# Kernel optimization log

Measured on AMD Instinct MI355X. Metric: run time of the kernel, lower is better.

The kernel has to match this reference:

```python
import jax, jax.numpy as jnp
import numpy as np

N, IN_DIM = 50000, 1024
E = 100000
NUM_REL = 40
HEADS, OUT_DIM = 4, 200
HID = HEADS * OUT_DIM  # 800
B = 8192
NEG_SLOPE = 0.2


def setup_inputs() -> dict:
    key = jax.random.key(0)
    ks = jax.random.split(key, 12)
    node_emb = jax.random.normal(ks[0], (N, IN_DIM), dtype=jnp.float32)
    # RelGAT learnable params
    W = jax.random.normal(ks[1], (IN_DIM, HID), dtype=jnp.float32) * (1.0 / np.sqrt(IN_DIM))
    bias = jnp.zeros((HID,), dtype=jnp.float32)
    a_src = jax.random.normal(ks[2], (HEADS, OUT_DIM), dtype=jnp.float32) * 0.1
    a_dst = jax.random.normal(ks[3], (HEADS, OUT_DIM), dtype=jnp.float32) * 0.1
    a_rel = jax.random.normal(ks[4], (HEADS, OUT_DIM), dtype=jnp.float32) * 0.1
    rel_feat = jax.random.normal(ks[5], (NUM_REL, HID), dtype=jnp.float32) * 0.1
    # DistMult scorer relation embeddings
    rel_emb = jax.random.normal(ks[6], (NUM_REL, HID), dtype=jnp.float32) * 0.1
    # Graph structure (constants)
    edge_index = jax.random.randint(ks[7], (2, E), 0, N, dtype=jnp.int64)
    edge_type = jax.random.randint(ks[8], (E,), 0, NUM_REL, dtype=jnp.int64)
    # Triple batch
    src_ids = jax.random.randint(ks[9], (B,), 0, N, dtype=jnp.int64)
    rel_ids = jax.random.randint(ks[10], (B,), 0, NUM_REL, dtype=jnp.int64)
    dst_ids = jax.random.randint(ks[11], (B,), 0, N, dtype=jnp.int64)
    return dict(node_emb=node_emb, W=W, bias=bias, a_src=a_src, a_dst=a_dst,
                a_rel=a_rel, rel_feat=rel_feat, rel_emb=rel_emb,
                edge_index=edge_index, edge_type=edge_type,
                src_ids=src_ids, rel_ids=rel_ids, dst_ids=dst_ids)


def _rel_gat(node_emb, W, bias, a_src, a_dst, a_rel, rel_feat, edge_index, edge_type):
    src, dst = edge_index[0], edge_index[1]
    h = (node_emb @ W).reshape(N, HEADS, OUT_DIM)          # [N,H,D]
    hs = h[src]                                            # [E,H,D] gather
    hd = h[dst]                                            # [E,H,D] gather
    r = rel_feat[edge_type].reshape(E, HEADS, OUT_DIM)     # [E,H,D]
    # relation-conditioned attention logits per head
    logits = (jnp.einsum('ehd,hd->eh', hs, a_src)
              + jnp.einsum('ehd,hd->eh', hd, a_dst)
              + jnp.einsum('ehd,hd->eh', r, a_rel))        # [E,H]
    logits = jax.nn.leaky_relu(logits, NEG_SLOPE)
    # segment softmax over incoming edges of each destination node
    seg_max = jax.ops.segment_max(logits, dst, num_segments=N)   # [N,H]
    e = jnp.exp(logits - seg_max[dst])                           # [E,H]
    denom = jax.ops.segment_sum(e, dst, num_segments=N)          # [N,H]
    alpha = e / denom[dst]                                       # [E,H]
    # weighted scatter-aggregate of source messages
    out = jax.ops.segment_sum(alpha[:, :, None] * hs, dst, num_segments=N)  # [N,H,D]
    return out.reshape(N, HID) + bias                            # dropout: eval mode (identity)


def reference(node_emb, W, bias, a_src, a_dst, a_rel, rel_feat, rel_emb,
              edge_index, edge_type, src_ids, rel_ids, dst_ids):
    refined = _rel_gat(node_emb, W, bias, a_src, a_dst, a_rel, rel_feat,
                       edge_index, edge_type)                # [N, HID]
    src_vec = refined[src_ids]                               # [B, HID]
    dst_vec = refined[dst_ids]                               # [B, HID]
    # DistMult: sum(s * r * d)
    scores = jnp.sum(src_vec * rel_emb[rel_ids] * dst_vec, axis=-1)  # [B]
    return scores
```

## Files before the change

kernel.cpp:

```cpp
#include <hip/hip_runtime.h>
#include <hip/hip_bf16.h>
#include <math.h>

#define NN 50000
#define IN_DIM 1024
#define EE 100000
#define NUM_REL 40
#define HEADS 4
#define OUT_D 200
#define HID 800
#define BB 8192
#define SLOT_CAP 16384
#define SRC_CAP 50176
#define WT_COLS 896

typedef __attribute__((ext_vector_type(8))) short short8;
typedef __attribute__((ext_vector_type(4))) float f32x4;

__device__ inline unsigned short f2bf(float f) {
    unsigned int u = __float_as_uint(f);
    u += 0x7FFF + ((u >> 16) & 1);
    return (unsigned short)(u >> 16);
}
__device__ inline float bf2f(unsigned short s) {
    return __uint_as_float(((unsigned int)s) << 16);
}
__device__ inline void gl2lds16(const unsigned short* g, unsigned short* l) {
    __builtin_amdgcn_global_load_lds(
        (const __attribute__((address_space(1))) void*)g,
        (__attribute__((address_space(3))) void*)l, 16, 0, 0);
}

#define INIT_BLOCKS 196
__global__ __launch_bounds__(256) void k_init_wa(int* slot_of_node, int* xrow_of_node,
                                                 int* deg, int* counters,
                                                 const float* W, const float* a_src,
                                                 const float* a_dst, const float* a_rel,
                                                 const float* rel_feat, float* Wa, float* prel) {
    int b = blockIdx.x;
    if (b < INIT_BLOCKS) {
        int i = b * 256 + threadIdx.x;
        if (i < NN) { slot_of_node[i] = -1; xrow_of_node[i] = -1; }
        if (i < SLOT_CAP) deg[i] = 0;
        if (i < 8) counters[i] = 0;
        return;
    }
    int wid = (b - INIT_BLOCKS) * 4 + (threadIdx.x >> 6);
    int lane = threadIdx.x & 63;
    if (wid >= IN_DIM * 8 + NUM_REL * HEADS) return;
    float acc = 0.f;
    int d = lane * 4;
    if (d < OUT_D) {
        const float* row;
        const float* a;
        if (wid < IN_DIM * 8) {
            int k = wid >> 3, c = wid & 7;
            int h = c & 3;
            row = W + (size_t)k * HID + h * OUT_D;
            a = ((c < 4) ? a_src : a_dst) + h * OUT_D;
        } else {
            int j = wid - IN_DIM * 8;
            int r = j >> 2, h = j & 3;
            row = rel_feat + (size_t)r * HID + h * OUT_D;
            a = a_rel + h * OUT_D;
        }
        float4 wv = *(const float4*)(row + d);
        float4 av = *(const float4*)(a + d);
        acc = wv.x * av.x + wv.y * av.y + wv.z * av.z + wv.w * av.w;
    }
    for (int off = 32; off; off >>= 1) acc += __shfl_down(acc, off, 64);
    if (lane == 0) {
        if (wid < IN_DIM * 8) Wa[wid] = acc;
        else prel[wid - IN_DIM * 8] = acc;
    }
}

__global__ void k_build_slots(const int* src_ids, const int* dst_ids,
                              int* slot_of_node, int* counters, int* scorelist) {
    int i = blockIdx.x * 256 + threadIdx.x;
    if (i >= 2 * BB) return;
    int n = (i < BB) ? src_ids[i] : dst_ids[i - BB];
    if (slot_of_node[n] == -1) {
        if (atomicCAS(&slot_of_node[n], -1, -2) == -1) {
            int s = atomicAdd(&counters[0], 1);
            slot_of_node[n] = s;
            scorelist[s] = n;
        }
    }
}

__global__ void k_edge0(const int* ei, const int* slot_of_node,
                        int* xrow_of_node, int* counters, int* rows, int* deg) {
    int e = blockIdx.x * 256 + threadIdx.x;
    if (e >= EE) return;
    int dn = ei[EE + e];
    int slot = slot_of_node[dn];
    if (slot < 0) return;
    int sn = ei[e];
    if (xrow_of_node[sn] == -1) {
        if (atomicCAS(&xrow_of_node[sn], -1, -2) == -1) {
            int t = atomicAdd(&counters[1], 1);
            rows[t] = sn;
            xrow_of_node[sn] = t;
        }
    }
    atomicAdd(&deg[slot], 1);
}

__global__ __launch_bounds__(256) void k_tail_scan(const int* scorelist, int* xrow_of_node,
                                                   int* counters, int* rows,
                                                   const int* deg, int* base, int* cursor) {
    int t = threadIdx.x;
    if (blockIdx.x == 0) {
        __shared__ int pref[257];
        int s = 0;
        const int4* dv = (const int4*)(deg + t * (SLOT_CAP / 256));
        for (int i = 0; i < SLOT_CAP / 256 / 4; ++i) {
            int4 v = dv[i];
            s += v.x + v.y + v.z + v.w;
        }
        pref[t + 1] = s;
        if (t == 0) pref[0] = 0;
        __syncthreads();
        if (t == 0)
            for (int i = 1; i <= 256; ++i) pref[i] += pref[i - 1];
        __syncthreads();
        int r = pref[t];
        for (int i = 0; i < SLOT_CAP / 256; ++i) {
            int idx = t * (SLOT_CAP / 256) + i;
            base[idx] = r;
            cursor[idx] = r;
            r += deg[idx];
        }
        return;
    }
    int i = (blockIdx.x - 1) * 256 + t;
    if (i >= counters[0]) return;
    int n = scorelist[i];
    if (xrow_of_node[n] < 0) {
        int tt = atomicAdd(&counters[3], 1);
        int xr = counters[1] + tt;
        xrow_of_node[n] = xr;
        rows[xr] = n;
    }
}

#define WT_BLOCKS 224
__global__ __launch_bounds__(256) void k_gather_wt(const float* x, const int* rows,
                                                   const int* counters, unsigned short* xg,
                                                   const float* W, const float* Wa,
                                                   unsigned short* Wt) {
    int t = threadIdx.x;
    if (blockIdx.x < WT_BLOCKS) {
        __shared__ float tile[64][65];
        int b = blockIdx.x;
        int k0 = (b & 15) * 64, c0 = (b >> 4) * 64;
        {
            int kk = t >> 2, cc = (t & 3) * 16;
            for (int i = 0; i < 16; ++i) {
                int c = c0 + cc + i;
                float v = 0.f;
                if (c < HID) v = W[(size_t)(k0 + kk) * HID + c];
                else if (c < HID + 8) v = Wa[(size_t)(k0 + kk) * 8 + (c - HID)];
                tile[cc + i][kk] = v;
            }
        }
        __syncthreads();
        {
            int cc = t >> 2, kk = (t & 3) * 16;
            unsigned short o[16];
            for (int i = 0; i < 16; ++i) o[i] = f2bf(tile[cc][kk + i]);
            *(short8*)(Wt + (size_t)(c0 + cc) * IN_DIM + k0 + kk) = *(short8*)o;
            *(short8*)(Wt + (size_t)(c0 + cc) * IN_DIM + k0 + kk + 8) = *(short8*)(o + 8);
        }
        return;
    }
    int nneed = counters[1] + counters[3];
    int gid = (blockIdx.x - WT_BLOCKS) * 256 + t;
    int row = gid >> 7;
    if (row >= nneed) return;
    int j = (gid & 127) * 8;
    int node = rows[row];
    const float* src = x + (size_t)node * IN_DIM + j;
    float4 a = *(const float4*)(src);
    float4 b = *(const float4*)(src + 4);
    unsigned short o[8] = {f2bf(a.x), f2bf(a.y), f2bf(a.z), f2bf(a.w),
                           f2bf(b.x), f2bf(b.y), f2bf(b.z), f2bf(b.w)};
    *(short8*)(xg + (size_t)row * IN_DIM + j) = *(short8*)o;
}

#define GBM 128
#define GBN 128
#define GBK 64
__global__ __launch_bounds__(256) void k_hgemm(const unsigned short* xg, const unsigned short* Wt,
                                               const int* counters, unsigned short* h_src,
                                               float* sS, float* sD) {
    int nsrc = counters[1];
    int nneed = nsrc + counters[3];
    int col0 = blockIdx.x * GBN;
    int row0 = blockIdx.y * GBM;
    int rowlim = (col0 == 768) ? nneed : nsrc;
    if (row0 >= rowlim) return;
    __shared__ unsigned short As[GBM * GBK];
    __shared__ unsigned short Bs[GBN * GBK];
    int t = threadIdx.x;
    int crow = ((t >> 6) << 4) + (t & 15), coff = ((t >> 4) & 3) << 3;
    const unsigned short* a0 = xg + (size_t)(row0 + crow) * IN_DIM + coff;
    const unsigned short* a1 = a0 + (size_t)64 * IN_DIM;
    const unsigned short* b0 = Wt + (size_t)(col0 + crow) * IN_DIM + coff;
    const unsigned short* b1 = b0 + (size_t)64 * IN_DIM;
    unsigned short* la0 = As + t * 8;
    unsigned short* la1 = As + (256 + t) * 8;
    unsigned short* la2 = As + (512 + t) * 8;
    unsigned short* la3 = As + (768 + t) * 8;
    unsigned short* lb0 = Bs + t * 8;
    unsigned short* lb1 = Bs + (256 + t) * 8;
    unsigned short* lb2 = Bs + (512 + t) * 8;
    unsigned short* lb3 = Bs + (768 + t) * 8;
    int w = t >> 6, lane = t & 63;
    int ga = (w >> 1) * 4, gb = (w & 1) * 4;
    int wr = (w >> 1) * 64, wc = (w & 1) * 64;
    int fm = lane & 15, fq = lane >> 4;
    f32x4 acc[4][4] = {};
    for (int k0 = 0; k0 < IN_DIM; k0 += GBK) {
        __syncthreads();
        gl2lds16(a0 + k0, la0);
        gl2lds16(a1 + k0, la1);
        gl2lds16(a0 + k0 + 32, la2);
        gl2lds16(a1 + k0 + 32, la3);
        gl2lds16(b0 + k0, lb0);
        gl2lds16(b1 + k0, lb1);
        gl2lds16(b0 + k0 + 32, lb2);
        gl2lds16(b1 + k0 + 32, lb3);
        __syncthreads();
#pragma unroll
        for (int s = 0; s < 2; ++s) {
            short8 af[4], bf[4];
#pragma unroll
            for (int i = 0; i < 4; ++i)
                af[i] = *(const short8*)&As[(s * 512 + (ga + i) * 64 + lane) * 8];
#pragma unroll
            for (int j = 0; j < 4; ++j)
                bf[j] = *(const short8*)&Bs[(s * 512 + (gb + j) * 64 + lane) * 8];
#pragma unroll
            for (int i = 0; i < 4; ++i)
#pragma unroll
                for (int j = 0; j < 4; ++j)
                    acc[i][j] = __builtin_amdgcn_mfma_f32_16x16x32_bf16(af[i], bf[j], acc[i][j], 0, 0, 0);
        }
    }
#pragma unroll
    for (int i = 0; i < 4; ++i) {
#pragma unroll
        for (int j = 0; j < 4; ++j) {
            int gcol = col0 + wc + j * 16 + fm;
            if (gcol >= HID + 8) continue;
#pragma unroll
            for (int r = 0; r < 4; ++r) {
                int grow = row0 + wr + i * 16 + fq * 4 + r;
                float v = acc[i][j][r];
                if (gcol < HID) {
                    if (grow < nsrc) h_src[(size_t)grow * HID + gcol] = f2bf(v);
                } else if (grow < nneed) {
                    int c = gcol - HID;
                    if (c < 4) sS[grow * 4 + c] = v;
                    else sD[grow * 4 + (c - 4)] = v;
                }
            }
        }
    }
}

__global__ void k_place(const int* ei, const int* etype, const int* slot_of_node,
                        const int* xrow_of_node, int* cursor,
                        const float* sS, const float* sD, const float* prel,
                        float* clogit, int* tlist) {
    int e = blockIdx.x * 256 + threadIdx.x;
    if (e >= EE) return;
    int dn = ei[EE + e];
    int slot = slot_of_node[dn];
    if (slot < 0) return;
    int sn = ei[e];
    int r = etype[e];
    int xs = xrow_of_node[sn];
    int xd = xrow_of_node[dn];
    int pos = atomicAdd(&cursor[slot], 1);
    tlist[pos] = xs;
    float4 lg;
    float* lp = (float*)&lg;
#pragma unroll
    for (int h = 0; h < 4; ++h) {
        float v = sS[xs * 4 + h] + sD[xd * 4 + h] + prel[r * 4 + h];
        lp[h] = v > 0.f ? v : 0.2f * v;
    }
    *(float4*)&clogit[(size_t)pos * 4] = lg;
}

__global__ __launch_bounds__(256) void k_aggregate(const int* counters, const int* base,
                                                   const int* deg, const int* tlist,
                                                   const float* clogit,
                                                   const unsigned short* h_src, const float* bias,
                                                   float* refined) {
    int b = blockIdx.x;
    if (b >= counters[0]) return;
    int beg = base[b], d = deg[b];
    __shared__ float m4[4], den4[4];
    __shared__ float alpha[64][4];
    __shared__ int tsl[64];
    int t = threadIdx.x;
    if (t < 4) {
        float m = -3e38f;
        for (int j = 0; j < d; ++j)
            m = fmaxf(m, clogit[(size_t)(beg + j) * 4 + t]);
        float s = 0.f;
        for (int j = 0; j < d; ++j)
            s += expf(clogit[(size_t)(beg + j) * 4 + t] - m);
        m4[t] = m;
        den4[t] = s;
    }
    __syncthreads();
    int h0 = t / 200, h1 = (t + 256) / 200, h2 = (t + 512) / 200;
    float acc0 = 0.f, acc1 = 0.f, acc2 = 0.f, acc3 = 0.f;
    for (int j0 = 0; j0 < d; j0 += 64) {
        int nc = min(64, d - j0);
        if (t < nc * 4) {
            int j = t >> 2, h = t & 3;
            alpha[j][h] = expf(clogit[(size_t)(beg + j0 + j) * 4 + h] - m4[h]) / den4[h];
            if (h == 0) tsl[j] = tlist[beg + j0 + j];
        }
        __syncthreads();
        for (int j = 0; j < nc; ++j) {
            const unsigned short* hr = h_src + (size_t)tsl[j] * HID;
            acc0 += alpha[j][h0] * bf2f(hr[t]);
            acc1 += alpha[j][h1] * bf2f(hr[t + 256]);
            acc2 += alpha[j][h2] * bf2f(hr[t + 512]);
            if (t < 32) acc3 += alpha[j][3] * bf2f(hr[768 + t]);
        }
        __syncthreads();
    }
    float* rr = refined + (size_t)b * HID;
    rr[t] = acc0 + bias[t];
    rr[t + 256] = acc1 + bias[t + 256];
    rr[t + 512] = acc2 + bias[t + 512];
    if (t < 32) rr[768 + t] = acc3 + bias[768 + t];
}

__global__ __launch_bounds__(256) void k_score(const int* src_ids, const int* rel_ids,
                                               const int* dst_ids, const int* slot_of_node,
                                               const float* rel_emb, const float* refined,
                                               float* out) {
    int gid = blockIdx.x * 256 + threadIdx.x;
    int b = gid >> 6;
    int lane = threadIdx.x & 63;
    if (b >= BB) return;
    int ss = slot_of_node[src_ids[b]];
    int ds = slot_of_node[dst_ids[b]];
    int r = rel_ids[b];
    const float* sv = refined + (size_t)ss * HID;
    const float* dv = refined + (size_t)ds * HID;
    const float* rv = rel_emb + (size_t)r * HID;
    float acc = 0.f;
    for (int c4 = lane; c4 < 200; c4 += 64) {
        float4 s = *(const float4*)(sv + c4 * 4);
        float4 dq = *(const float4*)(dv + c4 * 4);
        float4 rr = *(const float4*)(rv + c4 * 4);
        acc += s.x * rr.x * dq.x + s.y * rr.y * dq.y + s.z * rr.z * dq.z + s.w * rr.w * dq.w;
    }
    for (int off = 32; off; off >>= 1) acc += __shfl_down(acc, off, 64);
    if (lane == 0) out[b] = acc;
}

extern "C" void kernel_launch(void* const* d_in, const int* in_sizes, int n_in,
                              void* d_out, int out_size, void* d_ws, size_t ws_size,
                              hipStream_t stream) {
    const float* node_emb = (const float*)d_in[0];
    const float* W        = (const float*)d_in[1];
    const float* bias     = (const float*)d_in[2];
    const float* a_src    = (const float*)d_in[3];
    const float* a_dst    = (const float*)d_in[4];
    const float* a_rel    = (const float*)d_in[5];
    const float* rel_feat = (const float*)d_in[6];
    const float* rel_emb  = (const float*)d_in[7];
    const int* edge_index = (const int*)d_in[8];
    const int* edge_type  = (const int*)d_in[9];
    const int* src_ids    = (const int*)d_in[10];
    const int* rel_ids    = (const int*)d_in[11];
    const int* dst_ids    = (const int*)d_in[12];
    float* out = (float*)d_out;

    char* w = (char*)d_ws;
    auto alloc = [&](size_t bytes) -> void* {
        void* p = (void*)w;
        w += (bytes + 255) & ~(size_t)255;
        return p;
    };
    int* slot_of_node = (int*)alloc((size_t)NN * 4);
    int* xrow_of_node = (int*)alloc((size_t)NN * 4);
    int* scorelist    = (int*)alloc((size_t)SLOT_CAP * 4);
    int* rows         = (int*)alloc((size_t)NN * 4);
    int* counters     = (int*)alloc(256);
    int* deg          = (int*)alloc((size_t)SLOT_CAP * 4);
    int* base         = (int*)alloc((size_t)SLOT_CAP * 4);
    int* cursor       = (int*)alloc((size_t)SLOT_CAP * 4);
    int* tlist        = (int*)alloc((size_t)EE * 4);
    float* clogit = (float*)alloc((size_t)EE * 4 * 4);
    float* sS     = (float*)alloc((size_t)SRC_CAP * 4 * 4);
    float* sD     = (float*)alloc((size_t)SRC_CAP * 4 * 4);
    float* Wa     = (float*)alloc((size_t)IN_DIM * 8 * 4);
    float* prel   = (float*)alloc((size_t)NUM_REL * 4 * 4);
    unsigned short* xg    = (unsigned short*)alloc((size_t)SRC_CAP * IN_DIM * 2);
    unsigned short* Wt    = (unsigned short*)alloc((size_t)WT_COLS * IN_DIM * 2);
    unsigned short* h_src = (unsigned short*)alloc((size_t)SRC_CAP * HID * 2);
    float* refined = (float*)alloc((size_t)SLOT_CAP * HID * 4);

    int wa_blocks = (IN_DIM * 8 + NUM_REL * HEADS + 3) / 4;
    k_init_wa<<<INIT_BLOCKS + wa_blocks, 256, 0, stream>>>(
        slot_of_node, xrow_of_node, deg, counters,
        W, a_src, a_dst, a_rel, rel_feat, Wa, prel);
    k_build_slots<<<(2 * BB + 255) / 256, 256, 0, stream>>>(src_ids, dst_ids, slot_of_node,
                                                            counters, scorelist);
    k_edge0<<<(EE + 255) / 256, 256, 0, stream>>>(edge_index, slot_of_node,
                                                  xrow_of_node, counters, rows, deg);
    k_tail_scan<<<1 + SLOT_CAP / 256, 256, 0, stream>>>(scorelist, xrow_of_node, counters,
                                                        rows, deg, base, cursor);
    k_gather_wt<<<WT_BLOCKS + (NN * 128) / 256, 256, 0, stream>>>(
        node_emb, rows, counters, xg, W, Wa, Wt);
    dim3 ggrid(WT_COLS / GBN, (SRC_CAP + GBM - 1) / GBM);
    k_hgemm<<<ggrid, 256, 0, stream>>>(xg, Wt, counters, h_src, sS, sD);
    k_place<<<(EE + 255) / 256, 256, 0, stream>>>(edge_index, edge_type, slot_of_node,
                                                  xrow_of_node, cursor, sS, sD, prel,
                                                  clogit, tlist);
    k_aggregate<<<SLOT_CAP, 256, 0, stream>>>(counters, base, deg, tlist,
                                              clogit, h_src, bias, refined);
    k_score<<<(BB * 64 + 255) / 256, 256, 0, stream>>>(src_ids, rel_ids, dst_ids,
                                                       slot_of_node, rel_emb, refined, out);
}
```

Baseline: 519.0 us.

## Aggregate atomics per wave, grid-stride gather, and swizzle GEMM tile order

Replaces the per-thread atomicAdd on the global counters with a wave-level ballot and prefix scheme, so one lane reserves indices for the whole wave. This cuts contention on the counters in the slot-building, edge and tail kernels. The row gather now uses a fixed grid of 3584 blocks with a grid-stride loop instead of launching blocks for all 50000 possible rows. The GEMM block index is remapped into groups of 8 row tiles across all column tiles to improve L2 reuse of A tiles. Index assignment order becomes wave-ordered, which changes row numbering but not the final values.

```diff
diff --git a/kernel.cpp b/kernel.cpp
--- a/kernel.cpp
+++ b/kernel.cpp
@@ -29,6 +29,17 @@
     __builtin_amdgcn_global_load_lds(
         (const __attribute__((address_space(1))) void*)g,
         (__attribute__((address_space(3))) void*)l, 16, 0, 0);
+}
+
+__device__ inline int wave_compact(bool won, int* ctr) {
+    unsigned long long m = __ballot(won);
+    if (!m) return -1;
+    int lane = threadIdx.x & 63;
+    int leader = __ffsll((long long)m) - 1;
+    int base = 0;
+    if (lane == leader) base = atomicAdd(ctr, __popcll(m));
+    base = __shfl(base, leader, 64);
+    return won ? base + __popcll(m & ((1ull << lane) - 1)) : -1;
 }
 
 #define INIT_BLOCKS 196
@@ -78,33 +89,43 @@
 __global__ void k_build_slots(const int* src_ids, const int* dst_ids,
                               int* slot_of_node, int* counters, int* scorelist) {
     int i = blockIdx.x * 256 + threadIdx.x;
-    if (i >= 2 * BB) return;
-    int n = (i < BB) ? src_ids[i] : dst_ids[i - BB];
-    if (slot_of_node[n] == -1) {
-        if (atomicCAS(&slot_of_node[n], -1, -2) == -1) {
-            int s = atomicAdd(&counters[0], 1);
-            slot_of_node[n] = s;
-            scorelist[s] = n;
-        }
+    bool valid = i < 2 * BB;
+    int n = 0;
+    bool won = false;
+    if (valid) {
+        n = (i < BB) ? src_ids[i] : dst_ids[i - BB];
+        if (slot_of_node[n] == -1)
+            won = (atomicCAS(&slot_of_node[n], -1, -2) == -1);
+    }
+    int s = wave_compact(won, &counters[0]);
+    if (won) {
+        slot_of_node[n] = s;
+        scorelist[s] = n;
     }
 }
 
 __global__ void k_edge0(const int* ei, const int* slot_of_node,
                         int* xrow_of_node, int* counters, int* rows, int* deg) {
     int e = blockIdx.x * 256 + threadIdx.x;
-    if (e >= EE) return;
-    int dn = ei[EE + e];
-    int slot = slot_of_node[dn];
-    if (slot < 0) return;
-    int sn = ei[e];
-    if (xrow_of_node[sn] == -1) {
-        if (atomicCAS(&xrow_of_node[sn], -1, -2) == -1) {
-            int t = atomicAdd(&counters[1], 1);
-            rows[t] = sn;
-            xrow_of_node[sn] = t;
-        }
-    }
-    atomicAdd(&deg[slot], 1);
+    bool valid = e < EE;
+    int slot = -1, sn = 0;
+    if (valid) {
+        int dn = ei[EE + e];
+        slot = slot_of_node[dn];
+    }
+    bool surv = valid && slot >= 0;
+    bool won = false;
+    if (surv) {
+        sn = ei[e];
+        if (xrow_of_node[sn] == -1)
+            won = (atomicCAS(&xrow_of_node[sn], -1, -2) == -1);
+    }
+    int t = wave_compact(won, &counters[1]);
+    if (won) {
+        rows[t] = sn;
+        xrow_of_node[sn] = t;
+    }
+    if (surv) atomicAdd(&deg[slot], 1);
 }
 
 __global__ __launch_bounds__(256) void k_tail_scan(const int* scorelist, int* xrow_of_node,
@@ -135,10 +156,15 @@
         return;
     }
     int i = (blockIdx.x - 1) * 256 + t;
-    if (i >= counters[0]) return;
-    int n = scorelist[i];
-    if (xrow_of_node[n] < 0) {
-        int tt = atomicAdd(&counters[3], 1);
+    bool valid = i < counters[0];
+    int n = 0;
+    bool won = false;
+    if (valid) {
+        n = scorelist[i];
+        won = (xrow_of_node[n] < 0);
+    }
+    int tt = wave_compact(won, &counters[3]);
+    if (won) {
         int xr = counters[1] + tt;
         xrow_of_node[n] = xr;
         rows[xr] = n;
@@ -146,6 +172,7 @@
 }
 
 #define WT_BLOCKS 224
+#define GATHER_BLOCKS 3584
 __global__ __launch_bounds__(256) void k_gather_wt(const float* x, const int* rows,
                                                    const int* counters, unsigned short* xg,
                                                    const float* W, const float* Wa,
@@ -176,17 +203,19 @@
         return;
     }
     int nneed = counters[1] + counters[3];
-    int gid = (blockIdx.x - WT_BLOCKS) * 256 + t;
-    int row = gid >> 7;
-    if (row >= nneed) return;
-    int j = (gid & 127) * 8;
-    int node = rows[row];
-    const float* src = x + (size_t)node * IN_DIM + j;
-    float4 a = *(const float4*)(src);
-    float4 b = *(const float4*)(src + 4);
-    unsigned short o[8] = {f2bf(a.x), f2bf(a.y), f2bf(a.z), f2bf(a.w),
-                           f2bf(b.x), f2bf(b.y), f2bf(b.z), f2bf(b.w)};
-    *(short8*)(xg + (size_t)row * IN_DIM + j) = *(short8*)o;
+    int lim = nneed * 128;
+    for (int gid = (blockIdx.x - WT_BLOCKS) * 256 + t; gid < lim;
+         gid += GATHER_BLOCKS * 256) {
+        int row = gid >> 7;
+        int j = (gid & 127) * 8;
+        int node = rows[row];
+        const float* src = x + (size_t)node * IN_DIM + j;
+        float4 a = *(const float4*)(src);
+        float4 b = *(const float4*)(src + 4);
+        unsigned short o[8] = {f2bf(a.x), f2bf(a.y), f2bf(a.z), f2bf(a.w),
+                               f2bf(b.x), f2bf(b.y), f2bf(b.z), f2bf(b.w)};
+        *(short8*)(xg + (size_t)row * IN_DIM + j) = *(short8*)o;
+    }
 }
 
 #define GBM 128
@@ -197,8 +226,12 @@
                                                float* sS, float* sD) {
     int nsrc = counters[1];
     int nneed = nsrc + counters[3];
-    int col0 = blockIdx.x * GBN;
-    int row0 = blockIdx.y * GBM;
+    int lin = blockIdx.x + 7 * blockIdx.y;
+    int g = lin / 56, r = lin % 56;
+    int rowb = g * 8 + (r & 7);
+    int colb = r >> 3;
+    int col0 = colb * GBN;
+    int row0 = rowb * GBM;
     int rowlim = (col0 == 768) ? nneed : nsrc;
     if (row0 >= rowlim) return;
     __shared__ unsigned short As[GBM * GBK];
@@ -256,9 +289,9 @@
             int gcol = col0 + wc + j * 16 + fm;
             if (gcol >= HID + 8) continue;
 #pragma unroll
-            for (int r = 0; r < 4; ++r) {
-                int grow = row0 + wr + i * 16 + fq * 4 + r;
-                float v = acc[i][j][r];
+            for (int rr = 0; rr < 4; ++rr) {
+                int grow = row0 + wr + i * 16 + fq * 4 + rr;
+                float v = acc[i][j][rr];
                 if (gcol < HID) {
                     if (grow < nsrc) h_src[(size_t)grow * HID + gcol] = f2bf(v);
                 } else if (grow < nneed) {
@@ -423,7 +456,7 @@
                                                   xrow_of_node, counters, rows, deg);
     k_tail_scan<<<1 + SLOT_CAP / 256, 256, 0, stream>>>(scorelist, xrow_of_node, counters,
                                                         rows, deg, base, cursor);
-    k_gather_wt<<<WT_BLOCKS + (NN * 128) / 256, 256, 0, stream>>>(
+    k_gather_wt<<<WT_BLOCKS + GATHER_BLOCKS, 256, 0, stream>>>(
         node_emb, rows, counters, xg, W, Wa, Wt);
     dim3 ggrid(WT_COLS / GBN, (SRC_CAP + GBM - 1) / GBM);
     k_hgemm<<<ggrid, 256, 0, stream>>>(xg, Wt, counters, h_src, sS, sD);
```

Result: faster. 506.3 us (-2.5%).
